# Kernel tuning notes

Hardware: AMD Instinct MI355X
Metric: run time of the kernel (lower is better)

Reference implementation:

```python
import math
import jax, jax.numpy as jnp
import numpy as np

GROUPS = 8

def setup_inputs() -> dict:
    key = jax.random.key(0)
    ks = jax.random.split(key, 6)
    N, H, W, C = 8, 128, 128, 512
    s = 1.0 / math.sqrt(C)
    return {
        "x": jax.random.normal(ks[0], (N, H, W, C), dtype=jnp.float32),
        "Wq": jax.random.normal(ks[1], (C, C), dtype=jnp.float32) * s,
        "Wk": jax.random.normal(ks[2], (C, C), dtype=jnp.float32) * s,
        "Wv": jax.random.normal(ks[3], (C, C), dtype=jnp.float32) * s,
        "Wo": jax.random.normal(ks[4], (C, C), dtype=jnp.float32) * s,
        "bo": jnp.zeros((C,), dtype=jnp.float32),
    }

def reference(x, Wq, Wk, Wv, Wo, bo):
    # width=False: attend along H axis -> permute to [N, W, H, C]
    x = jnp.transpose(x, (0, 2, 1, 3))
    N, W, H, C = x.shape
    g = GROUPS
    gp = C // g  # group_planes (head dim)
    xr = x.reshape(N * W, H, C)
    # torch nn.Linear: y = x @ W^T
    q = (xr @ Wq.T).reshape(N * W, H, g, gp)
    k = (xr @ Wk.T).reshape(N * W, H, g, gp)
    v = (xr @ Wv.T).reshape(N * W, H, g, gp)
    attn = jnp.einsum('nigc,njgc->nijg', q, k / math.sqrt(gp))
    attn = jax.nn.softmax(attn, axis=2)
    out = jnp.einsum('nijg,njgc->nigc', attn, v)
    out = out.reshape(N * W, H, C)
    out = out @ Wo.T + bo
    out = out.reshape(N, W, H, C)
    return jnp.transpose(out, (0, 2, 1, 3))
```

## Files before the change

kernel.cpp:

```cpp
#include <hip/hip_runtime.h>
#include <stdint.h>


typedef __attribute__((ext_vector_type(4))) float f32x4;
typedef __attribute__((ext_vector_type(8))) short bf16x8;
typedef unsigned short u16;
typedef unsigned int u32;

#define CBAR() asm volatile("" ::: "memory")
#define SBAR() do { CBAR(); __builtin_amdgcn_s_barrier(); CBAR(); } while(0)
#define LGKM0() do { asm volatile("s_waitcnt lgkmcnt(0)" ::: "memory"); __builtin_amdgcn_sched_barrier(0); } while(0)
#define LGKMW() asm volatile("s_waitcnt lgkmcnt(0)" ::: "memory")
#define VMC(n) asm volatile("s_waitcnt vmcnt(" #n ")" ::: "memory")

static __device__ __forceinline__ u16 f2bf(float f){
    union { float f; u32 u; } v; v.f = f;
    u32 r = v.u + 0x7fffu + ((v.u >> 16) & 1u);
    return (u16)(r >> 16);
}

static __device__ __forceinline__ void gload16(const void* g, void* l){
    __builtin_amdgcn_global_load_lds((const __attribute__((address_space(1))) void*)g,
                                     (__attribute__((address_space(3))) void*)l, 16, 0, 0);
}

__global__ void k_wconv(const float* __restrict__ Wq, const float* __restrict__ Wk,
                        const float* __restrict__ Wv, const float* __restrict__ Wo,
                        u16* __restrict__ Wcat, u16* __restrict__ Wob){
    int e = (blockIdx.x * 256 + threadIdx.x) * 4;
    if (e < 1536*512) {
        int row = e >> 9, col = e & 511;
        const float* s = (row < 512) ? (Wq + row*512)
                        : (row < 1024 ? Wk + (row-512)*512 : Wv + (row-1024)*512);
        float4 v = *(const float4*)(s + col);
        ushort4 o = { f2bf(v.x), f2bf(v.y), f2bf(v.z), f2bf(v.w) };
        *(ushort4*)(Wcat + e) = o;
    } else {
        int e2 = e - 1536*512;
        float4 v = *(const float4*)(Wo + e2);
        ushort4 o = { f2bf(v.x), f2bf(v.y), f2bf(v.z), f2bf(v.w) };
        *(ushort4*)(Wob + e2) = o;
    }
}

__global__ void k_xconv(const float* __restrict__ x, u16* __restrict__ xb, int n0){
    int t = blockIdx.x * 256 + threadIdx.x;
    int ml = t >> 6;
    int c0 = (t & 63) << 3;
    int nl = ml >> 7, h = ml & 127;
    int n = n0 + nl, nb = n >> 7, w = n & 127;
    const float* src = x + (size_t)((nb*128 + h)*128 + w) * 512 + c0;
    float4 a = *(const float4*)(src);
    float4 b = *(const float4*)(src + 4);
    uint4 o;
    o.x = (u32)f2bf(a.x) | ((u32)f2bf(a.y) << 16);
    o.y = (u32)f2bf(a.z) | ((u32)f2bf(a.w) << 16);
    o.z = (u32)f2bf(b.x) | ((u32)f2bf(b.y) << 16);
    o.w = (u32)f2bf(b.z) | ((u32)f2bf(b.w) << 16);
    *(uint4*)(xb + (size_t)ml*512 + c0) = o;
}

template<int NCOL>
__global__ __launch_bounds__(512, 2) void k_gemm4(const u16* __restrict__ A, const u16* __restrict__ B,
                                                  u16* __restrict__ Cout, int nrow, int planesz){
    extern __shared__ char smc[];
    const int tid = threadIdx.x;
    const int wid = tid >> 6, lane = tid & 63, lg = lane >> 4, li = lane & 15;
    const int wm = wid >> 2, wn = wid & 3;
    const int bid = blockIdx.x;
    const int xcd = bid & 7, l = bid >> 3;
    const int row_tile = xcd * (nrow >> 3) + l / NCOL;
    const int col_tile = l % NCOL;
    const int m0 = row_tile * 256, nn0 = col_tile * 256;

    const char* baseA[2]; const char* baseB[2]; int dstR[2];
    #pragma unroll
    for (int i = 0; i < 2; ++i) {
        int R = wid*32 + i*16;
        int r = R + (lane >> 2);
        int cq = (lane & 3) ^ ((r >> 1) & 3);
        baseA[i] = (const char*)(A + (size_t)(m0 + r)*512) + cq*16;
        baseB[i] = (const char*)(B + (size_t)(nn0 + r)*512) + cq*16;
        dstR[i] = R;
    }
    auto stageA = [&](int st){
        char* sl = smc + (st & 3)*32768;
        #pragma unroll
        for (int i = 0; i < 2; ++i) gload16(baseA[i] + st*64, sl + dstR[i]*64);
    };
    auto stageB = [&](int st){
        char* sl = smc + (st & 3)*32768 + 16384;
        #pragma unroll
        for (int i = 0; i < 2; ++i) gload16(baseB[i] + st*64, sl + dstR[i]*64);
    };

    f32x4 acc[8][4];
    #pragma unroll
    for (int i = 0; i < 8; ++i)
        #pragma unroll
        for (int j = 0; j < 4; ++j)
            acc[i][j] = f32x4{0.f, 0.f, 0.f, 0.f};

    stageA(0); stageB(0);
    stageA(1); stageB(1);
    stageA(2); stageB(2);
    VMC(8);
    SBAR();

    bf16x8 af[4], bfr[4];
    for (int t = 0; t < 16; ++t) {
        char* sl = smc + (t & 3)*32768;
        #pragma unroll
        for (int f = 0; f < 4; ++f) {
            int ra = wm*128 + f*16 + li;
            af[f] = *(const bf16x8*)(sl + ra*64 + (((lg ^ (ra >> 1)) & 3) << 4));
        }
        #pragma unroll
        for (int f = 0; f < 4; ++f) {
            int rb = wn*64 + f*16 + li;
            bfr[f] = *(const bf16x8*)(sl + 16384 + rb*64 + (((lg ^ (rb >> 1)) & 3) << 4));
        }
        if (t < 13) stageA(t + 3);
        SBAR(); LGKM0();
        __builtin_amdgcn_s_setprio(1);
        #pragma unroll
        for (int fi = 0; fi < 4; ++fi)
            #pragma unroll
            for (int fj = 0; fj < 4; ++fj)
                acc[fi][fj] = __builtin_amdgcn_mfma_f32_16x16x32_bf16(af[fi], bfr[fj], acc[fi][fj], 0, 0, 0);
        __builtin_amdgcn_s_setprio(0);
        SBAR();
        #pragma unroll
        for (int f = 0; f < 4; ++f) {
            int ra = wm*128 + (4 + f)*16 + li;
            af[f] = *(const bf16x8*)(sl + ra*64 + (((lg ^ (ra >> 1)) & 3) << 4));
        }
        if (t < 13) stageB(t + 3);
        SBAR(); LGKM0();
        __builtin_amdgcn_s_setprio(1);
        #pragma unroll
        for (int fi = 0; fi < 4; ++fi)
            #pragma unroll
            for (int fj = 0; fj < 4; ++fj)
                acc[4 + fi][fj] = __builtin_amdgcn_mfma_f32_16x16x32_bf16(af[fi], bfr[fj], acc[4 + fi][fj], 0, 0, 0);
        __builtin_amdgcn_s_setprio(0);
        if (t < 13)      { VMC(8); }
        else if (t == 13){ VMC(4); }
        else if (t == 14){ VMC(0); }
        SBAR();
    }

    u16* Cp = Cout + (size_t)(nn0 >> 9) * planesz;
    const int cb = (nn0 & 511) + wn*64;
    #pragma unroll
    for (int mf = 0; mf < 8; ++mf)
        #pragma unroll
        for (int nf = 0; nf < 4; ++nf)
            #pragma unroll
            for (int r = 0; r < 4; ++r) {
                int row = m0 + wm*128 + mf*16 + lg*4 + r;
                int col = cb + nf*16 + li;
                Cp[(size_t)row*512 + col] = f2bf(acc[mf][nf][r]);
            }
}

__global__ __launch_bounds__(512, 2) void k_fused(const u16* __restrict__ Qpl, const u16* __restrict__ Kpl,
                                                  const u16* __restrict__ Vpl, const u16* __restrict__ Wob,
                                                  const float* __restrict__ bias, float* __restrict__ out,
                                                  int n0, int cnd8){
    extern __shared__ char sm[];
    const int tid = threadIdx.x;
    const int wv = tid >> 6, lane = tid & 63, lg = lane >> 4, li = lane & 15;
    const int bid = blockIdx.x;
    const int nlL = (bid & 7)*cnd8 + (bid >> 3);
    const int n = n0 + nlL, nb = n >> 7, w = n & 127;

    char* const QB = sm + 131072;
    char* const KB = sm + 131072 + 16384;
    char* const PB = sm + 131072 + wv*4096;
    char* const SB = sm + 131072;

    const int vj = tid & 127, vch = tid >> 7;
    const size_t rowbase = (size_t)nlL * 128;

    auto issueQK = [&](int g){
        #pragma unroll
        for (int t = 0; t < 2; ++t) {
            int i = t*64 + (tid >> 3);
            int cq = (tid & 7) ^ (i & 7);
            gload16(Qpl + (rowbase + i)*512 + g*64 + cq*8, QB + t*8192 + tid*16);
            gload16(Kpl + (rowbase + i)*512 + g*64 + cq*8, KB + t*8192 + tid*16);
        }
    };

    uint4 va, vb;
    auto issueV = [&](int g){
        const u16* src = Vpl + (rowbase + vj)*512 + g*64 + vch*16;
        va = *(const uint4*)(src);
        vb = *(const uint4*)(src + 8);
    };

    issueQK(0);
    issueV(0);
    __builtin_amdgcn_sched_barrier(0);

    for (int g = 0; g < 8; ++g) {
        char* OG = sm + g*16384;

        VMC(0);
        SBAR();

        f32x4 s8[8];
        #pragma unroll
        for (int tj = 0; tj < 8; ++tj) s8[tj] = f32x4{0.f,0.f,0.f,0.f};
        #pragma unroll
        for (int ks = 0; ks < 2; ++ks) {
            int i = wv*16 + li;
            bf16x8 qf = *(const bf16x8*)(QB + i*128 + ((ks*64 + lg*16) ^ ((li & 7) << 4)));
            #pragma unroll
            for (int tj = 0; tj < 8; ++tj) {
                int j = tj*16 + li;
                bf16x8 kf = *(const bf16x8*)(KB + j*128 + ((ks*64 + lg*16) ^ ((li & 7) << 4)));
                s8[tj] = __builtin_amdgcn_mfma_f32_16x16x32_bf16(qf, kf, s8[tj], 0, 0, 0);
            }
        }

        {
            u32 wd[8] = {va.x, va.y, va.z, va.w, vb.x, vb.y, vb.z, vb.w};
            #pragma unroll
            for (int cc = 0; cc < 16; ++cc) {
                int c = vch*16 + cc;
                u16 val = (cc & 1) ? (u16)(wd[cc >> 1] >> 16) : (u16)(wd[cc >> 1] & 0xffffu);
                *(u16*)(OG + c*256 + ((vj*2) ^ ((c & 7) << 4))) = val;
            }
        }

        SBAR();

        #pragma unroll
        for (int r = 0; r < 4; ++r) {
            int ir = lg*4 + r;
            float mx = -1e30f;
            #pragma unroll
            for (int tj = 0; tj < 8; ++tj) mx = fmaxf(mx, s8[tj][r]);
            #pragma unroll
            for (int off = 1; off < 16; off <<= 1) mx = fmaxf(mx, __shfl_xor(mx, off, 64));
            float p[8]; float sum = 0.f;
            #pragma unroll
            for (int tj = 0; tj < 8; ++tj) { p[tj] = __expf((s8[tj][r] - mx)*0.125f); sum += p[tj]; }
            #pragma unroll
            for (int off = 1; off < 16; off <<= 1) sum += __shfl_xor(sum, off, 64);
            float inv = 1.0f / sum;
            #pragma unroll
            for (int tj = 0; tj < 8; ++tj) {
                int j = tj*16 + li;
                *(u16*)(PB + ir*256 + ((j*2) ^ ((ir & 7) << 4))) = f2bf(p[tj]*inv);
            }
        }

        LGKMW();
        SBAR();

        f32x4 o4[4];
        #pragma unroll
        for (int tc = 0; tc < 4; ++tc) o4[tc] = f32x4{0.f,0.f,0.f,0.f};
        #pragma unroll
        for (int ks = 0; ks < 4; ++ks) {
            bf16x8 pf = *(const bf16x8*)(PB + li*256 + ((ks*64 + lg*16) ^ ((li & 7) << 4)));
            #pragma unroll
            for (int tc = 0; tc < 4; ++tc) {
                int c = tc*16 + li;
                bf16x8 vf = *(const bf16x8*)(OG + c*256 + ((ks*64 + lg*16) ^ ((c & 7) << 4)));
                o4[tc] = __builtin_amdgcn_mfma_f32_16x16x32_bf16(pf, vf, o4[tc], 0, 0, 0);
            }
        }

        SBAR();

        if (g < 7) {
            issueQK(g + 1);
            issueV(g + 1);
            __builtin_amdgcn_sched_barrier(0);
        }

        #pragma unroll
        for (int tc = 0; tc < 4; ++tc)
            #pragma unroll
            for (int r = 0; r < 4; ++r) {
                int i = wv*16 + lg*4 + r;
                int c = tc*16 + li;
                *(u16*)(OG + i*128 + ((c*2) ^ ((i & 7) << 4))) = f2bf(o4[tc][r]);
            }
    }

    LGKMW();

    float br[32];
    #pragma unroll
    for (int cf = 0; cf < 32; ++cf) br[cf] = bias[cf*16 + li];

    f32x4 y[32];
    #pragma unroll
    for (int cf = 0; cf < 32; ++cf) y[cf] = f32x4{0.f,0.f,0.f,0.f};

    for (int kc = 0; kc < 16; ++kc) {
        #pragma unroll
        for (int p = 0; p < 4; ++p) {
            int co = p*128 + (tid >> 2);
            int cq = (tid & 3) ^ ((co >> 1) & 3);
            gload16(Wob + (size_t)co*512 + kc*32 + cq*8, SB + p*8192 + tid*16);
        }
        VMC(0); LGKMW();
        SBAR();

        int i = wv*16 + li;
        bf16x8 af = *(const bf16x8*)(sm + (kc >> 1)*16384 + i*128 +
                                     (((kc & 1)*64 + lg*16) ^ ((li & 7) << 4)));
        __builtin_amdgcn_s_setprio(1);
        #pragma unroll
        for (int cf = 0; cf < 32; ++cf) {
            int co = cf*16 + li;
            bf16x8 bf = *(const bf16x8*)(SB + co*64 + ((lg << 4) ^ (((co >> 1) & 3) << 4)));
            y[cf] = __builtin_amdgcn_mfma_f32_16x16x32_bf16(af, bf, y[cf], 0, 0, 0);
        }
        __builtin_amdgcn_s_setprio(0);
        SBAR();
    }

    #pragma unroll
    for (int cf = 0; cf < 32; ++cf)
        #pragma unroll
        for (int r = 0; r < 4; ++r) {
            int i = wv*16 + lg*4 + r;
            int co = cf*16 + li;
            out[((size_t)(nb*128 + i)*128 + w)*512 + co] = y[cf][r] + br[cf];
        }
}

extern "C" void kernel_launch(void* const* d_in, const int* in_sizes, int n_in,
                              void* d_out, int out_size, void* d_ws, size_t ws_size,
                              hipStream_t stream){
    const float* x  = (const float*)d_in[0];
    const float* Wq = (const float*)d_in[1];
    const float* Wk = (const float*)d_in[2];
    const float* Wv = (const float*)d_in[3];
    const float* Wo = (const float*)d_in[4];
    const float* bo = (const float*)d_in[5];

    char* ws = (char*)d_ws;
    u16* Wcat = (u16*)ws;
    u16* Wob  = Wcat + 1536*512;

    int CN = 1024;
    while (CN > 128 && (size_t)2097152 + (size_t)CN*524288 > ws_size) CN >>= 1;
    u16* xb   = (u16*)(ws + 2097152);
    u16* QKV2 = xb + (size_t)CN*128*512;
    int planesz = CN*128*512;

    hipFuncSetAttribute((const void*)&k_gemm4<6>,
                        hipFuncAttributeMaxDynamicSharedMemorySize, 131072);
    hipFuncSetAttribute((const void*)&k_fused,
                        hipFuncAttributeMaxDynamicSharedMemorySize, 163840);

    k_wconv<<<1024, 256, 0, stream>>>(Wq, Wk, Wv, Wo, Wcat, Wob);
    int nch = 1024 / CN;
    for (int ch = 0; ch < nch; ++ch) {
        int n0 = ch * CN;
        int nrow = (CN * 128) / 256;
        k_xconv<<<CN*32, 256, 0, stream>>>(x, xb, n0);
        k_gemm4<6><<<nrow*6, 512, 131072, stream>>>(xb, Wcat, QKV2, nrow, planesz);
        k_fused<<<CN, 512, 163840, stream>>>(QKV2, QKV2 + planesz, QKV2 + 2*(size_t)planesz,
                                             Wob, bo, (float*)d_out, n0, CN/8);
    }
}
```

Measured before the change: 653.3 us.

## Register-stage Q/K and Wo tile loads to overlap global fetches with MFMA

Replaces the direct global-to-LDS async loads of Q/K tiles with register-staged loads. They are issued earlier, after the QK^T MFMAs, and written to LDS after the PV stage. This lets the next group's fetch overlap with softmax and PV compute instead of stalling on vmcnt at the loop top. The Wo projection loop is double-buffered through registers the same way, so the next chunk's fetch overlaps the current chunk's MFMAs. The trade-off is extra VGPR pressure from the staging registers, alongside the already large 32-accumulator array, which may reduce occupancy or cause spills.

```diff
diff --git a/kernel.cpp b/kernel.cpp
--- a/kernel.cpp
+++ b/kernel.cpp
@@ -183,32 +183,37 @@
     const int vj = tid & 127, vch = tid >> 7;
     const size_t rowbase = (size_t)nlL * 128;
 
+    const int qi = tid >> 3, qc = tid & 7;
+    const u16* const Qsrc = Qpl + rowbase*512 + (size_t)qi*512 + qc*8;
+    const u16* const Ksrc = Kpl + rowbase*512 + (size_t)qi*512 + qc*8;
+    const int qdst = qi*128 + ((qc ^ (qi & 7)) << 4);
+
+    uint4 rq0, rq1, rk0, rk1, va, vb;
     auto issueQK = [&](int g){
-        #pragma unroll
-        for (int t = 0; t < 2; ++t) {
-            int i = t*64 + (tid >> 3);
-            int cq = (tid & 7) ^ (i & 7);
-            gload16(Qpl + (rowbase + i)*512 + g*64 + cq*8, QB + t*8192 + tid*16);
-            gload16(Kpl + (rowbase + i)*512 + g*64 + cq*8, KB + t*8192 + tid*16);
-        }
-    };
-
-    uint4 va, vb;
+        rq0 = *(const uint4*)(Qsrc + g*64);
+        rq1 = *(const uint4*)(Qsrc + 64*512 + g*64);
+        rk0 = *(const uint4*)(Ksrc + g*64);
+        rk1 = *(const uint4*)(Ksrc + 64*512 + g*64);
+    };
+    auto writeQK = [&](){
+        *(uint4*)(QB + qdst)        = rq0;
+        *(uint4*)(QB + 8192 + qdst) = rq1;
+        *(uint4*)(KB + qdst)        = rk0;
+        *(uint4*)(KB + 8192 + qdst) = rk1;
+    };
     auto issueV = [&](int g){
         const u16* src = Vpl + (rowbase + vj)*512 + g*64 + vch*16;
         va = *(const uint4*)(src);
         vb = *(const uint4*)(src + 8);
     };
 
-    issueQK(0);
-    issueV(0);
-    __builtin_amdgcn_sched_barrier(0);
+    issueQK(0); issueV(0);
+    writeQK();
+    LGKMW();
+    SBAR();
 
     for (int g = 0; g < 8; ++g) {
         char* OG = sm + g*16384;
-
-        VMC(0);
-        SBAR();
 
         f32x4 s8[8];
         #pragma unroll
@@ -234,6 +239,7 @@
                 *(u16*)(OG + c*256 + ((vj*2) ^ ((c & 7) << 4))) = val;
             }
         }
+        if (g < 7) { issueV(g + 1); issueQK(g + 1); }
 
         SBAR();
 
@@ -277,11 +283,7 @@
 
         SBAR();
 
-        if (g < 7) {
-            issueQK(g + 1);
-            issueV(g + 1);
-            __builtin_amdgcn_sched_barrier(0);
-        }
+        if (g < 7) writeQK();
 
         #pragma unroll
         for (int tc = 0; tc < 4; ++tc)
@@ -291,28 +293,31 @@
                 int c = tc*16 + li;
                 *(u16*)(OG + i*128 + ((c*2) ^ ((i & 7) << 4))) = f2bf(o4[tc][r]);
             }
-    }
-
-    LGKMW();
-
-    float br[32];
-    #pragma unroll
-    for (int cf = 0; cf < 32; ++cf) br[cf] = bias[cf*16 + li];
+
+        LGKMW();
+        SBAR();
+    }
+
+    const int oco = tid >> 2, och = tid & 3;
+    uint4 w4a[4], w4b[4];
+    auto issueW = [&](uint4* W, int kc){
+        #pragma unroll
+        for (int p = 0; p < 4; ++p)
+            W[p] = *(const uint4*)(Wob + (size_t)(p*128 + oco)*512 + kc*32 + och*8);
+    };
+    auto writeW = [&](const uint4* W){
+        #pragma unroll
+        for (int p = 0; p < 4; ++p) {
+            int co = p*128 + oco;
+            *(uint4*)(SB + p*8192 + oco*64 + ((och ^ ((co >> 1) & 3)) << 4)) = W[p];
+        }
+    };
 
     f32x4 y[32];
     #pragma unroll
     for (int cf = 0; cf < 32; ++cf) y[cf] = f32x4{0.f,0.f,0.f,0.f};
 
-    for (int kc = 0; kc < 16; ++kc) {
-        #pragma unroll
-        for (int p = 0; p < 4; ++p) {
-            int co = p*128 + (tid >> 2);
-            int cq = (tid & 3) ^ ((co >> 1) & 3);
-            gload16(Wob + (size_t)co*512 + kc*32 + cq*8, SB + p*8192 + tid*16);
-        }
-        VMC(0); LGKMW();
-        SBAR();
-
+    auto mfmaW = [&](int kc){
         int i = wv*16 + li;
         bf16x8 af = *(const bf16x8*)(sm + (kc >> 1)*16384 + i*128 +
                                      (((kc & 1)*64 + lg*16) ^ ((li & 7) << 4)));
@@ -324,17 +329,31 @@
             y[cf] = __builtin_amdgcn_mfma_f32_16x16x32_bf16(af, bf, y[cf], 0, 0, 0);
         }
         __builtin_amdgcn_s_setprio(0);
-        SBAR();
-    }
-
-    #pragma unroll
-    for (int cf = 0; cf < 32; ++cf)
+    };
+
+    issueW(w4a, 0);
+    for (int kc2 = 0; kc2 < 16; kc2 += 2) {
+        writeW(w4a);
+        issueW(w4b, kc2 + 1);
+        LGKMW(); SBAR();
+        mfmaW(kc2);
+        SBAR();
+        writeW(w4b);
+        if (kc2 + 2 < 16) issueW(w4a, kc2 + 2);
+        LGKMW(); SBAR();
+        mfmaW(kc2 + 1);
+        SBAR();
+    }
+
+    #pragma unroll
+    for (int cf = 0; cf < 32; ++cf) {
+        float bv = bias[cf*16 + li];
         #pragma unroll
         for (int r = 0; r < 4; ++r) {
             int i = wv*16 + lg*4 + r;
-            int co = cf*16 + li;
-            out[((size_t)(nb*128 + i)*128 + w)*512 + co] = y[cf][r] + br[cf];
-        }
+            out[((size_t)(nb*128 + i)*128 + w)*512 + cf*16 + li] = y[cf][r] + bv;
+        }
+    }
 }
 
 extern "C" void kernel_launch(void* const* d_in, const int* in_sizes, int n_in,
```

Result: slower. 728.3 us (+11.5%).
